# Optimization experiments

Measured on AMD Instinct MI355X. Metric: run time of the kernel, lower is better.

Reference implementation:

```python
import jax, jax.numpy as jnp
import numpy as np

DIM = 1024
HEADS = 16
HEAD_DIM = 64
INNER = HEADS * HEAD_DIM  # 1024
B, N = 4, 2048
EPS = 1e-5


def setup_inputs() -> dict:
    key = jax.random.key(0)
    ks = jax.random.split(key, 5)
    x = jax.random.normal(ks[0], (B, N, DIM), dtype=jnp.float32)
    w_qkv = jax.random.normal(ks[1], (DIM, 3 * INNER), dtype=jnp.float32) * (DIM ** -0.5)
    w_out = jax.random.normal(ks[2], (INNER, DIM), dtype=jnp.float32) * (INNER ** -0.5)
    b_out = jax.random.normal(ks[3], (DIM,), dtype=jnp.float32) * 0.01
    ln_gamma = jnp.ones((DIM,), dtype=jnp.float32)
    ln_beta = jnp.zeros((DIM,), dtype=jnp.float32)
    return {"x": x, "w_qkv": w_qkv, "w_out": w_out, "b_out": b_out,
            "ln_gamma": ln_gamma, "ln_beta": ln_beta}


def reference(x, w_qkv, w_out, b_out, ln_gamma, ln_beta):
    scale = HEAD_DIM ** -0.5
    qkv = x @ w_qkv  # [b, n, 3*inner]
    q, k, v = jnp.split(qkv, 3, axis=-1)
    q = q * scale
    # [b, n, h*d] -> [b, h, n, d]
    def to_heads(t):
        b, n, _ = t.shape
        return t.reshape(b, n, HEADS, HEAD_DIM).transpose(0, 2, 1, 3)
    q, k, v = to_heads(q), to_heads(k), to_heads(v)
    scores = jnp.einsum('bhid,bhjd->bhij', q, k)
    attn = jax.nn.softmax(scores, axis=-1)  # max-subtraction (detached) is internal
    out = jnp.einsum('bhij,bhjd->bhid', attn, v)
    out = out.transpose(0, 2, 1, 3).reshape(x.shape[0], x.shape[1], INNER)
    out = out @ w_out + b_out
    # LayerNorm over last dim
    mu = out.mean(axis=-1, keepdims=True)
    var = out.var(axis=-1, keepdims=True)
    out = (out - mu) * jax.lax.rsqrt(var + EPS)
    return out * ln_gamma + ln_beta
```

## Files before the change

kernel.cpp:

```cpp
#include <hip/hip_runtime.h>


typedef __bf16 bf16;
typedef __bf16 bf16x4 __attribute__((ext_vector_type(4)));
typedef __bf16 bf16x8 __attribute__((ext_vector_type(8)));
typedef float f32x4 __attribute__((ext_vector_type(4)));
typedef float f32x16 __attribute__((ext_vector_type(16)));
typedef unsigned int u32x2 __attribute__((ext_vector_type(2)));
typedef unsigned int u32x4 __attribute__((ext_vector_type(4)));

#define QSCALE_LOG2E 0.18033688011112042f

#define GLOAD_LDS16(gp, lp)                                                   \
  __builtin_amdgcn_global_load_lds(                                           \
      (const __attribute__((address_space(1))) unsigned int*)(const void*)(gp), \
      (__attribute__((address_space(3))) unsigned int*)(void*)(lp), 16, 0, 0)

__device__ __forceinline__ float fexp2(float x) {
#if __has_builtin(__builtin_amdgcn_exp2f)
  return __builtin_amdgcn_exp2f(x);
#else
  return __expf(x * 0.6931471805599453f);
#endif
}

__device__ __forceinline__ unsigned pack2t(float lo, float hi) {
  return __builtin_amdgcn_perm(__float_as_uint(hi), __float_as_uint(lo), 0x07060302u);
}

__global__ __launch_bounds__(256) void cvt_k(const float* __restrict__ in,
                                             bf16* __restrict__ out) {
  const size_t i = ((size_t)blockIdx.x * 256 + threadIdx.x) * 8;
  float4 a = *(const float4*)(in + i);
  float4 b = *(const float4*)(in + i + 4);
  bf16x8 o = {(bf16)a.x, (bf16)a.y, (bf16)a.z, (bf16)a.w,
              (bf16)b.x, (bf16)b.y, (bf16)b.z, (bf16)b.w};
  *(bf16x8*)(out + i) = o;
}

__global__ __launch_bounds__(256) void transpose_k(const float* __restrict__ in,
                                                   bf16* __restrict__ out,
                                                   int Kd, int Nd) {
  __shared__ bf16 t[32][36];
  const int n0 = blockIdx.x * 32, k0 = blockIdx.y * 32;
  const int r = threadIdx.x >> 3, c4 = (threadIdx.x & 7) * 4;
  float4 v = *(const float4*)(in + (size_t)(k0 + r) * Nd + n0 + c4);
  t[c4 + 0][r] = (bf16)v.x; t[c4 + 1][r] = (bf16)v.y;
  t[c4 + 2][r] = (bf16)v.z; t[c4 + 3][r] = (bf16)v.w;
  __syncthreads();
  bf16x4 o = *(const bf16x4*)&t[r][c4];
  *(bf16x4*)(out + (size_t)(n0 + r) * Kd + k0 + c4) = o;
}

template <bool QKV>
__global__ __launch_bounds__(256) void gemm2(const bf16* __restrict__ A,
                                             const bf16* __restrict__ Bt,
                                             bf16* __restrict__ C,
                                             bf16* __restrict__ Vt) {
  __shared__ bf16 As[128][32];
  __shared__ bf16 Bs[128][32];
  const int tid = threadIdx.x;
  const int l = tid & 63, w = tid >> 6;
  const int g = l >> 4, q = l & 15;
  const int wm = w >> 1, wn = w & 1;
  const int m0 = blockIdx.x * 128, n0 = blockIdx.y * 128;
  const int lr = l >> 2, lc = (l & 3) * 8;

  f32x4 acc[4][4] = {};

  for (int k0 = 0; k0 < 1024; k0 += 32) {
    __syncthreads();
#pragma unroll
    for (int i = 0; i < 2; i++) {
      const int c = w + i * 4;
      GLOAD_LDS16(A + (size_t)(m0 + c * 16 + lr) * 1024 + k0 + lc, &As[c * 16][0]);
      GLOAD_LDS16(Bt + (size_t)(n0 + c * 16 + lr) * 1024 + k0 + lc, &Bs[c * 16][0]);
    }
    __syncthreads();

    bf16x8 af[4], bfr[4];
#pragma unroll
    for (int mi = 0; mi < 4; mi++)
      af[mi] = *(const bf16x8*)&As[wm * 64 + mi * 16 + q][g * 8];
#pragma unroll
    for (int ni = 0; ni < 4; ni++)
      bfr[ni] = *(const bf16x8*)&Bs[wn * 64 + ni * 16 + q][g * 8];
#pragma unroll
    for (int mi = 0; mi < 4; mi++)
#pragma unroll
      for (int ni = 0; ni < 4; ni++)
        acc[mi][ni] = __builtin_amdgcn_mfma_f32_16x16x32_bf16(af[mi], bfr[ni], acc[mi][ni], 0, 0, 0);
  }

  if (QKV && n0 >= 2048) {
#pragma unroll
    for (int mi = 0; mi < 4; mi++)
#pragma unroll
      for (int ni = 0; ni < 4; ni++) {
        const int vcol = n0 - 2048 + wn * 64 + ni * 16 + q;
        const int h = vcol >> 6, d = vcol & 63;
        const int t0 = m0 + wm * 64 + mi * 16 + g * 4;
        const int b = t0 >> 11, n = t0 & 2047;
        bf16x4 o = {(bf16)acc[mi][ni][0], (bf16)acc[mi][ni][1],
                    (bf16)acc[mi][ni][2], (bf16)acc[mi][ni][3]};
        *(bf16x4*)(Vt + ((size_t)(b * 16 + h) * 64 + d) * 2048 + n) = o;
      }
  } else {
    const int ldc = QKV ? 2048 : 1024;
    const float s = (QKV && n0 < 1024) ? QSCALE_LOG2E : 1.0f;
#pragma unroll
    for (int mi = 0; mi < 4; mi++)
#pragma unroll
      for (int ni = 0; ni < 4; ni++) {
        const int col = n0 + wn * 64 + ni * 16 + q;
#pragma unroll
        for (int r = 0; r < 4; r++) {
          const int row = m0 + wm * 64 + mi * 16 + g * 4 + r;
          C[(size_t)row * ldc + col] = (bf16)(acc[mi][ni][r] * s);
        }
      }
  }
}

__global__ __launch_bounds__(256, 3) void attn_k(const bf16* __restrict__ qk,
                                                 const bf16* __restrict__ vt,
                                                 bf16* __restrict__ aout) {
  __shared__ bf16 Ks[3][64][64];
  __shared__ bf16 Vs[3][64][64];
  const int tid = threadIdx.x;
  const int l = tid & 63, w = tid >> 6;
  const int q = l & 31, hi = l >> 5, q7 = q & 7;

  const int flat = blockIdx.x;
  const int logical = (flat & 7) * 128 + (flat >> 3);
  const int qt = logical & 15, bh = logical >> 4;
  const int h = bh & 15, b = bh >> 4;
  const int qbase = qt * 128 + w * 32;

  const bf16* Kg = qk + (size_t)(b * 2048) * 2048 + 1024 + h * 64;
  const bf16* Vg = vt + ((size_t)(b * 16 + h) * 64) * 2048;

  bf16x8 qf[4];
  {
    const bf16* Qr = qk + (size_t)(b * 2048 + qbase + q) * 2048 + h * 64 + hi * 8;
#pragma unroll
    for (int i = 0; i < 4; i++) qf[i] = *(const bf16x8*)(Qr + i * 16);
  }

  const int r0 = tid >> 3, sp0 = ((tid & 7) ^ (r0 & 7)) * 8;
  const int ub = (tid >> 6) << 9;
#define STAGE_KV(buf, kt)                                                       \
  do {                                                                          \
    bf16* kd = &Ks[buf][0][0];                                                  \
    bf16* vd = &Vs[buf][0][0];                                                  \
    GLOAD_LDS16(Kg + (size_t)((kt) + r0) * 2048 + sp0, kd + ub);                \
    GLOAD_LDS16(Vg + (size_t)r0 * 2048 + (kt) + sp0, vd + ub);                  \
    GLOAD_LDS16(Kg + (size_t)((kt) + 32 + r0) * 2048 + sp0, kd + 2048 + ub);    \
    GLOAD_LDS16(Vg + (size_t)(32 + r0) * 2048 + (kt) + sp0, vd + 2048 + ub);    \
  } while (0)

  f32x16 oacc[2] = {};
  float lsA = 0.f, lsB = 0.f;

  STAGE_KV(0, 0);
  STAGE_KV(1, 64);
  int cur = 0, nxt2 = 2;

  for (int kt = 0; kt < 2048; kt += 64) {
    if (kt == 2048 - 64) {
      asm volatile("s_waitcnt vmcnt(0)" ::: "memory");
    } else {
      asm volatile("s_waitcnt vmcnt(4)" ::: "memory");
    }
    __builtin_amdgcn_sched_barrier(0);
    __builtin_amdgcn_s_barrier();

    if (kt + 128 < 2048) STAGE_KV(nxt2, kt + 128);

    const char* Kb = (const char*)&Ks[cur][0][0];
    const char* Vb = (const char*)&Vs[cur][0][0];

    f32x16 st[2];
    __builtin_amdgcn_s_setprio(1);
#pragma unroll
    for (int s = 0; s < 2; s++) {
      f32x16 acc = {};
#pragma unroll
      for (int i = 0; i < 4; i++) {
        bf16x8 kf = *(const bf16x8*)(Kb + (s * 32 + q) * 128 + (((2 * i + hi) ^ q7) << 4));
        acc = __builtin_amdgcn_mfma_f32_32x32x16_bf16(kf, qf[i], acc, 0, 0, 0);
      }
      st[s] = acc;
    }
    __builtin_amdgcn_s_setprio(0);

    bf16x8 vfr[2][4];
#pragma unroll
    for (int dblk = 0; dblk < 2; dblk++)
#pragma unroll
      for (int t = 0; t < 4; t++)
        vfr[dblk][t] = *(const bf16x8*)(Vb + (dblk * 32 + q) * 128 + (((2 * t + hi) ^ q7) << 4));

#pragma unroll
    for (int r = 0; r < 16; r++) { st[0][r] = fexp2(st[0][r]); lsA += st[0][r]; }
#pragma unroll
    for (int r = 0; r < 16; r++) { st[1][r] = fexp2(st[1][r]); lsB += st[1][r]; }

    bf16x8 pfrag[4];
#pragma unroll
    for (int s = 0; s < 2; s++)
#pragma unroll
      for (int ks = 0; ks < 2; ks++) {
        const unsigned a0 = pack2t(st[s][8 * ks + 0], st[s][8 * ks + 1]);
        const unsigned a1 = pack2t(st[s][8 * ks + 2], st[s][8 * ks + 3]);
        const unsigned b0 = pack2t(st[s][8 * ks + 4], st[s][8 * ks + 5]);
        const unsigned b1 = pack2t(st[s][8 * ks + 6], st[s][8 * ks + 7]);
        u32x2 w0 = __builtin_amdgcn_permlane32_swap(a0, b0, false, false);
        u32x2 w1 = __builtin_amdgcn_permlane32_swap(a1, b1, false, false);
        u32x4 bw = {w0[0], w1[0], w0[1], w1[1]};
        pfrag[2 * s + ks] = __builtin_bit_cast(bf16x8, bw);
      }

    __builtin_amdgcn_s_setprio(1);
#pragma unroll
    for (int dblk = 0; dblk < 2; dblk++)
#pragma unroll
      for (int t = 0; t < 4; t++)
        oacc[dblk] = __builtin_amdgcn_mfma_f32_32x32x16_bf16(vfr[dblk][t], pfrag[t],
                                                             oacc[dblk], 0, 0, 0);
    __builtin_amdgcn_s_setprio(0);

    cur = (cur == 2) ? 0 : cur + 1;
    nxt2 = (nxt2 == 2) ? 0 : nxt2 + 1;
  }

  float lsum = lsA + lsB;
  {
    u32x2 t2 = __builtin_amdgcn_permlane32_swap(__float_as_uint(lsum),
                                                __float_as_uint(lsum), false, false);
    lsum = __uint_as_float(t2[0]) + __uint_as_float(t2[1]);
  }
  const float inv = 1.f / lsum;
  bf16* orow = aout + (size_t)(b * 2048 + qbase + q) * 1024 + h * 64 + hi * 4;
#pragma unroll
  for (int dblk = 0; dblk < 2; dblk++)
#pragma unroll
    for (int rg = 0; rg < 4; rg++) {
      bf16x4 o = {(bf16)(oacc[dblk][4 * rg + 0] * inv), (bf16)(oacc[dblk][4 * rg + 1] * inv),
                  (bf16)(oacc[dblk][4 * rg + 2] * inv), (bf16)(oacc[dblk][4 * rg + 3] * inv)};
      *(bf16x4*)(orow + dblk * 32 + rg * 8) = o;
    }
#undef STAGE_KV
}

__global__ __launch_bounds__(256) void ln_k(const bf16* __restrict__ proj,
                                            const float* __restrict__ bo,
                                            const float* __restrict__ gam,
                                            const float* __restrict__ bet,
                                            float* __restrict__ out) {
  const int row = blockIdx.x, tid = threadIdx.x;
  const int l = tid & 63, w = tid >> 6;
  bf16x4 pv = *(const bf16x4*)(proj + (size_t)row * 1024 + tid * 4);
  float4 bv = *(const float4*)(bo + tid * 4);
  float v0 = (float)pv[0] + bv.x, v1 = (float)pv[1] + bv.y;
  float v2 = (float)pv[2] + bv.z, v3 = (float)pv[3] + bv.w;
  float s = v0 + v1 + v2 + v3;
  float ss = v0 * v0 + v1 * v1 + v2 * v2 + v3 * v3;
#pragma unroll
  for (int off = 32; off > 0; off >>= 1) {
    s += __shfl_xor(s, off);
    ss += __shfl_xor(ss, off);
  }
  __shared__ float red[8];
  if (l == 0) { red[w] = s; red[w + 4] = ss; }
  __syncthreads();
  const float S = red[0] + red[1] + red[2] + red[3];
  const float SS = red[4] + red[5] + red[6] + red[7];
  const float mean = S * (1.f / 1024.f);
  const float var = SS * (1.f / 1024.f) - mean * mean;
  const float rs = rsqrtf(var + 1e-5f);
  float4 gv = *(const float4*)(gam + tid * 4);
  float4 btv = *(const float4*)(bet + tid * 4);
  float4 o;
  o.x = (v0 - mean) * rs * gv.x + btv.x;
  o.y = (v1 - mean) * rs * gv.y + btv.y;
  o.z = (v2 - mean) * rs * gv.z + btv.z;
  o.w = (v3 - mean) * rs * gv.w + btv.w;
  *(float4*)(out + (size_t)row * 1024 + tid * 4) = o;
}

extern "C" void kernel_launch(void* const* d_in, const int* in_sizes, int n_in,
                              void* d_out, int out_size, void* d_ws, size_t ws_size,
                              hipStream_t stream) {
  const float* x      = (const float*)d_in[0];
  const float* w_qkv  = (const float*)d_in[1];
  const float* w_out  = (const float*)d_in[2];
  const float* b_out  = (const float*)d_in[3];
  const float* gamma  = (const float*)d_in[4];
  const float* beta   = (const float*)d_in[5];
  float* out = (float*)d_out;

  char* ws = (char*)d_ws;
  bf16* xbf   = (bf16*)(ws);
  bf16* wqkvT = (bf16*)(ws + 16777216);
  bf16* woutT = (bf16*)(ws + 23068672);
  bf16* qkbuf = (bf16*)(ws + 25165824);
  bf16* vt    = (bf16*)(ws + 58720256);
  bf16* aout  = xbf;
  bf16* proj  = vt;

  dim3 blk(256);
  cvt_k<<<4096, blk, 0, stream>>>(x, xbf);
  transpose_k<<<dim3(96, 32), blk, 0, stream>>>(w_qkv, wqkvT, 1024, 3072);
  transpose_k<<<dim3(32, 32), blk, 0, stream>>>(w_out, woutT, 1024, 1024);
  gemm2<true><<<dim3(64, 24), blk, 0, stream>>>(xbf, wqkvT, qkbuf, vt);
  attn_k<<<1024, blk, 0, stream>>>(qkbuf, vt, aout);
  gemm2<false><<<dim3(64, 8), blk, 0, stream>>>(aout, woutT, proj, nullptr);
  ln_k<<<8192, blk, 0, stream>>>(proj, b_out, gamma, beta, out);
}
```

Measured before the change: 201.8 us.

## Double-buffer 128-key attention tiles and swizzle GEMM block order across XCDs

```diff
diff --git a/kernel.cpp b/kernel.cpp
--- a/kernel.cpp
+++ b/kernel.cpp
@@ -63,7 +63,10 @@
   const int l = tid & 63, w = tid >> 6;
   const int g = l >> 4, q = l & 15;
   const int wm = w >> 1, wn = w & 1;
-  const int m0 = blockIdx.x * 128, n0 = blockIdx.y * 128;
+  const int nwg = (int)(gridDim.x * gridDim.y);
+  const int flat = (int)(blockIdx.y * gridDim.x + blockIdx.x);
+  const int swz = (flat & 7) * (nwg >> 3) + (flat >> 3);
+  const int m0 = (swz & 63) * 128, n0 = (swz >> 6) * 128;
   const int lr = l >> 2, lc = (l & 3) * 8;
 
   f32x4 acc[4][4] = {};
@@ -125,8 +128,8 @@
 __global__ __launch_bounds__(256, 3) void attn_k(const bf16* __restrict__ qk,
                                                  const bf16* __restrict__ vt,
                                                  bf16* __restrict__ aout) {
-  __shared__ bf16 Ks[3][64][64];
-  __shared__ bf16 Vs[3][64][64];
+  __shared__ bf16 Ks[2][2][64][64];
+  __shared__ bf16 Vs[2][2][64][64];
   const int tid = threadIdx.x;
   const int l = tid & 63, w = tid >> 6;
   const int q = l & 31, hi = l >> 5, q7 = q & 7;
@@ -149,89 +152,88 @@
 
   const int r0 = tid >> 3, sp0 = ((tid & 7) ^ (r0 & 7)) * 8;
   const int ub = (tid >> 6) << 9;
-#define STAGE_KV(buf, kt)                                                       \
+#define STAGE(buf, kt)                                                          \
   do {                                                                          \
-    bf16* kd = &Ks[buf][0][0];                                                  \
-    bf16* vd = &Vs[buf][0][0];                                                  \
-    GLOAD_LDS16(Kg + (size_t)((kt) + r0) * 2048 + sp0, kd + ub);                \
-    GLOAD_LDS16(Vg + (size_t)r0 * 2048 + (kt) + sp0, vd + ub);                  \
-    GLOAD_LDS16(Kg + (size_t)((kt) + 32 + r0) * 2048 + sp0, kd + 2048 + ub);    \
-    GLOAD_LDS16(Vg + (size_t)(32 + r0) * 2048 + (kt) + sp0, vd + 2048 + ub);    \
+    bf16* k0 = &Ks[buf][0][0][0]; bf16* k1 = &Ks[buf][1][0][0];                 \
+    bf16* v0 = &Vs[buf][0][0][0]; bf16* v1 = &Vs[buf][1][0][0];                 \
+    GLOAD_LDS16(Kg + (size_t)((kt) + r0) * 2048 + sp0,           k0 + ub);      \
+    GLOAD_LDS16(Kg + (size_t)((kt) + 32 + r0) * 2048 + sp0,      k0 + 2048 + ub);\
+    GLOAD_LDS16(Kg + (size_t)((kt) + 64 + r0) * 2048 + sp0,      k1 + ub);      \
+    GLOAD_LDS16(Kg + (size_t)((kt) + 96 + r0) * 2048 + sp0,      k1 + 2048 + ub);\
+    GLOAD_LDS16(Vg + (size_t)r0 * 2048 + (kt) + sp0,             v0 + ub);      \
+    GLOAD_LDS16(Vg + (size_t)(32 + r0) * 2048 + (kt) + sp0,      v0 + 2048 + ub);\
+    GLOAD_LDS16(Vg + (size_t)r0 * 2048 + (kt) + 64 + sp0,        v1 + ub);      \
+    GLOAD_LDS16(Vg + (size_t)(32 + r0) * 2048 + (kt) + 64 + sp0, v1 + 2048 + ub);\
   } while (0)
 
   f32x16 oacc[2] = {};
   float lsA = 0.f, lsB = 0.f;
 
-  STAGE_KV(0, 0);
-  STAGE_KV(1, 64);
-  int cur = 0, nxt2 = 2;
-
-  for (int kt = 0; kt < 2048; kt += 64) {
-    if (kt == 2048 - 64) {
-      asm volatile("s_waitcnt vmcnt(0)" ::: "memory");
-    } else {
-      asm volatile("s_waitcnt vmcnt(4)" ::: "memory");
-    }
+#define SUBTILE(Kb, Vb)                                                         \
+  do {                                                                          \
+    f32x16 st[2];                                                               \
+    __builtin_amdgcn_s_setprio(1);                                              \
+    _Pragma("unroll")                                                           \
+    for (int s = 0; s < 2; s++) {                                               \
+      f32x16 acc = {};                                                          \
+      _Pragma("unroll")                                                         \
+      for (int i = 0; i < 4; i++) {                                             \
+        bf16x8 kf = *(const bf16x8*)((Kb) + (s * 32 + q) * 128 +                \
+                                     (((2 * i + hi) ^ q7) << 4));               \
+        acc = __builtin_amdgcn_mfma_f32_32x32x16_bf16(kf, qf[i], acc, 0, 0, 0); \
+      }                                                                         \
+      st[s] = acc;                                                              \
+    }                                                                           \
+    __builtin_amdgcn_s_setprio(0);                                              \
+    bf16x8 vfr[2][4];                                                           \
+    _Pragma("unroll")                                                           \
+    for (int dblk = 0; dblk < 2; dblk++)                                        \
+      _Pragma("unroll")                                                         \
+      for (int t = 0; t < 4; t++)                                               \
+        vfr[dblk][t] = *(const bf16x8*)((Vb) + (dblk * 32 + q) * 128 +          \
+                                        (((2 * t + hi) ^ q7) << 4));            \
+    _Pragma("unroll")                                                           \
+    for (int r = 0; r < 16; r++) { st[0][r] = fexp2(st[0][r]); lsA += st[0][r]; }\
+    _Pragma("unroll")                                                           \
+    for (int r = 0; r < 16; r++) { st[1][r] = fexp2(st[1][r]); lsB += st[1][r]; }\
+    bf16x8 pfrag[4];                                                            \
+    _Pragma("unroll")                                                           \
+    for (int s = 0; s < 2; s++)                                                 \
+      _Pragma("unroll")                                                         \
+      for (int ks = 0; ks < 2; ks++) {                                          \
+        const unsigned a0 = pack2t(st[s][8 * ks + 0], st[s][8 * ks + 1]);       \
+        const unsigned a1 = pack2t(st[s][8 * ks + 2], st[s][8 * ks + 3]);       \
+        const unsigned b0 = pack2t(st[s][8 * ks + 4], st[s][8 * ks + 5]);       \
+        const unsigned b1 = pack2t(st[s][8 * ks + 6], st[s][8 * ks + 7]);       \
+        u32x2 w0 = __builtin_amdgcn_permlane32_swap(a0, b0, false, false);      \
+        u32x2 w1 = __builtin_amdgcn_permlane32_swap(a1, b1, false, false);      \
+        u32x4 bw = {w0[0], w1[0], w0[1], w1[1]};                                \
+        pfrag[2 * s + ks] = __builtin_bit_cast(bf16x8, bw);                     \
+      }                                                                         \
+    __builtin_amdgcn_s_setprio(1);                                              \
+    _Pragma("unroll")                                                           \
+    for (int dblk = 0; dblk < 2; dblk++)                                        \
+      _Pragma("unroll")                                                         \
+      for (int t = 0; t < 4; t++)                                               \
+        oacc[dblk] = __builtin_amdgcn_mfma_f32_32x32x16_bf16(vfr[dblk][t],      \
+                                            pfrag[t], oacc[dblk], 0, 0, 0);     \
+    __builtin_amdgcn_s_setprio(0);                                              \
+  } while (0)
+
+  STAGE(0, 0);
+  int cur = 0;
+
+  for (int kt = 0; kt < 2048; kt += 128) {
+    asm volatile("s_waitcnt vmcnt(0)" ::: "memory");
     __builtin_amdgcn_sched_barrier(0);
     __builtin_amdgcn_s_barrier();
 
-    if (kt + 128 < 2048) STAGE_KV(nxt2, kt + 128);
-
-    const char* Kb = (const char*)&Ks[cur][0][0];
-    const char* Vb = (const char*)&Vs[cur][0][0];
-
-    f32x16 st[2];
-    __builtin_amdgcn_s_setprio(1);
-#pragma unroll
-    for (int s = 0; s < 2; s++) {
-      f32x16 acc = {};
-#pragma unroll
-      for (int i = 0; i < 4; i++) {
-        bf16x8 kf = *(const bf16x8*)(Kb + (s * 32 + q) * 128 + (((2 * i + hi) ^ q7) << 4));
-        acc = __builtin_amdgcn_mfma_f32_32x32x16_bf16(kf, qf[i], acc, 0, 0, 0);
-      }
-      st[s] = acc;
-    }
-    __builtin_amdgcn_s_setprio(0);
-
-    bf16x8 vfr[2][4];
-#pragma unroll
-    for (int dblk = 0; dblk < 2; dblk++)
-#pragma unroll
-      for (int t = 0; t < 4; t++)
-        vfr[dblk][t] = *(const bf16x8*)(Vb + (dblk * 32 + q) * 128 + (((2 * t + hi) ^ q7) << 4));
-
-#pragma unroll
-    for (int r = 0; r < 16; r++) { st[0][r] = fexp2(st[0][r]); lsA += st[0][r]; }
-#pragma unroll
-    for (int r = 0; r < 16; r++) { st[1][r] = fexp2(st[1][r]); lsB += st[1][r]; }
-
-    bf16x8 pfrag[4];
-#pragma unroll
-    for (int s = 0; s < 2; s++)
-#pragma unroll
-      for (int ks = 0; ks < 2; ks++) {
-        const unsigned a0 = pack2t(st[s][8 * ks + 0], st[s][8 * ks + 1]);
-        const unsigned a1 = pack2t(st[s][8 * ks + 2], st[s][8 * ks + 3]);
-        const unsigned b0 = pack2t(st[s][8 * ks + 4], st[s][8 * ks + 5]);
-        const unsigned b1 = pack2t(st[s][8 * ks + 6], st[s][8 * ks + 7]);
-        u32x2 w0 = __builtin_amdgcn_permlane32_swap(a0, b0, false, false);
-        u32x2 w1 = __builtin_amdgcn_permlane32_swap(a1, b1, false, false);
-        u32x4 bw = {w0[0], w1[0], w0[1], w1[1]};
-        pfrag[2 * s + ks] = __builtin_bit_cast(bf16x8, bw);
-      }
-
-    __builtin_amdgcn_s_setprio(1);
-#pragma unroll
-    for (int dblk = 0; dblk < 2; dblk++)
-#pragma unroll
-      for (int t = 0; t < 4; t++)
-        oacc[dblk] = __builtin_amdgcn_mfma_f32_32x32x16_bf16(vfr[dblk][t], pfrag[t],
-                                                             oacc[dblk], 0, 0, 0);
-    __builtin_amdgcn_s_setprio(0);
-
-    cur = (cur == 2) ? 0 : cur + 1;
-    nxt2 = (nxt2 == 2) ? 0 : nxt2 + 1;
+    if (kt + 128 < 2048) STAGE(cur ^ 1, kt + 128);
+
+    SUBTILE((const char*)&Ks[cur][0][0][0], (const char*)&Vs[cur][0][0][0]);
+    SUBTILE((const char*)&Ks[cur][1][0][0], (const char*)&Vs[cur][1][0][0]);
+
+    cur ^= 1;
   }
 
   float lsum = lsA + lsB;
@@ -250,7 +252,8 @@
                   (bf16)(oacc[dblk][4 * rg + 2] * inv), (bf16)(oacc[dblk][4 * rg + 3] * inv)};
       *(bf16x4*)(orow + dblk * 32 + rg * 8) = o;
     }
-#undef STAGE_KV
+#undef SUBTILE
+#undef STAGE
 }
 
 __global__ __launch_bounds__(256) void ln_k(const bf16* __restrict__ proj,
```

New measurement: 215.6 us. 1.07x slower.

## Software-pipeline QK^T of next KV tile with softmax and PV of current

Applied to the files above, without the earlier changes.

```diff
diff --git a/kernel.cpp b/kernel.cpp
--- a/kernel.cpp
+++ b/kernel.cpp
@@ -159,79 +159,104 @@
     GLOAD_LDS16(Vg + (size_t)(32 + r0) * 2048 + (kt) + sp0, vd + 2048 + ub);    \
   } while (0)
 
+#define QKT(buf, sA, sB)                                                        \
+  do {                                                                          \
+    const char* Kb_ = (const char*)&Ks[buf][0][0];                              \
+    __builtin_amdgcn_s_setprio(1);                                              \
+    {                                                                           \
+      f32x16 a_ = {};                                                           \
+      _Pragma("unroll")                                                         \
+      for (int i = 0; i < 4; i++) {                                             \
+        bf16x8 kf = *(const bf16x8*)(Kb_ + q * 128 + (((2 * i + hi) ^ q7) << 4));\
+        a_ = __builtin_amdgcn_mfma_f32_32x32x16_bf16(kf, qf[i], a_, 0, 0, 0);   \
+      }                                                                         \
+      sA = a_;                                                                  \
+    }                                                                           \
+    {                                                                           \
+      f32x16 a_ = {};                                                           \
+      _Pragma("unroll")                                                         \
+      for (int i = 0; i < 4; i++) {                                             \
+        bf16x8 kf = *(const bf16x8*)(Kb_ + (32 + q) * 128 +                     \
+                                     (((2 * i + hi) ^ q7) << 4));               \
+        a_ = __builtin_amdgcn_mfma_f32_32x32x16_bf16(kf, qf[i], a_, 0, 0, 0);   \
+      }                                                                         \
+      sB = a_;                                                                  \
+    }                                                                           \
+    __builtin_amdgcn_s_setprio(0);                                              \
+  } while (0)
+
   f32x16 oacc[2] = {};
   float lsA = 0.f, lsB = 0.f;
 
   STAGE_KV(0, 0);
   STAGE_KV(1, 64);
-  int cur = 0, nxt2 = 2;
-
+  asm volatile("s_waitcnt vmcnt(4)" ::: "memory");
+  __builtin_amdgcn_sched_barrier(0);
+  __builtin_amdgcn_s_barrier();
+
+  f32x16 s0, s1;
+  QKT(0, s0, s1);
+
+  int cur = 0;
   for (int kt = 0; kt < 2048; kt += 64) {
-    if (kt == 2048 - 64) {
-      asm volatile("s_waitcnt vmcnt(0)" ::: "memory");
-    } else {
-      asm volatile("s_waitcnt vmcnt(4)" ::: "memory");
-    }
+    const int nbuf = (cur == 2) ? 0 : cur + 1;
+    const int sbuf = (nbuf == 2) ? 0 : nbuf + 1;
+
+    asm volatile("s_waitcnt vmcnt(0)" ::: "memory");
     __builtin_amdgcn_sched_barrier(0);
     __builtin_amdgcn_s_barrier();
 
-    if (kt + 128 < 2048) STAGE_KV(nxt2, kt + 128);
-
-    const char* Kb = (const char*)&Ks[cur][0][0];
+    if (kt + 128 < 2048) STAGE_KV(sbuf, kt + 128);
+
+    f32x16 n0v, n1v;
+    QKT(nbuf, n0v, n1v);
+
+#pragma unroll
+    for (int r = 0; r < 16; r++) { s0[r] = fexp2(s0[r]); lsA += s0[r]; }
+#pragma unroll
+    for (int r = 0; r < 16; r++) { s1[r] = fexp2(s1[r]); lsB += s1[r]; }
+
+    bf16x8 pfrag[4];
+#pragma unroll
+    for (int ks = 0; ks < 2; ks++) {
+      const unsigned a0 = pack2t(s0[8 * ks + 0], s0[8 * ks + 1]);
+      const unsigned a1 = pack2t(s0[8 * ks + 2], s0[8 * ks + 3]);
+      const unsigned b0 = pack2t(s0[8 * ks + 4], s0[8 * ks + 5]);
+      const unsigned b1 = pack2t(s0[8 * ks + 6], s0[8 * ks + 7]);
+      u32x2 w0 = __builtin_amdgcn_permlane32_swap(a0, b0, false, false);
+      u32x2 w1 = __builtin_amdgcn_permlane32_swap(a1, b1, false, false);
+      u32x4 bw = {w0[0], w1[0], w0[1], w1[1]};
+      pfrag[ks] = __builtin_bit_cast(bf16x8, bw);
+    }
+#pragma unroll
+    for (int ks = 0; ks < 2; ks++) {
+      const unsigned a0 = pack2t(s1[8 * ks + 0], s1[8 * ks + 1]);
+      const unsigned a1 = pack2t(s1[8 * ks + 2], s1[8 * ks + 3]);
+      const unsigned b0 = pack2t(s1[8 * ks + 4], s1[8 * ks + 5]);
+      const unsigned b1 = pack2t(s1[8 * ks + 6], s1[8 * ks + 7]);
+      u32x2 w0 = __builtin_amdgcn_permlane32_swap(a0, b0, false, false);
+      u32x2 w1 = __builtin_amdgcn_permlane32_swap(a1, b1, false, false);
+      u32x4 bw = {w0[0], w1[0], w0[1], w1[1]};
+      pfrag[2 + ks] = __builtin_bit_cast(bf16x8, bw);
+    }
+
     const char* Vb = (const char*)&Vs[cur][0][0];
-
-    f32x16 st[2];
     __builtin_amdgcn_s_setprio(1);
 #pragma unroll
-    for (int s = 0; s < 2; s++) {
-      f32x16 acc = {};
-#pragma unroll
-      for (int i = 0; i < 4; i++) {
-        bf16x8 kf = *(const bf16x8*)(Kb + (s * 32 + q) * 128 + (((2 * i + hi) ^ q7) << 4));
-        acc = __builtin_amdgcn_mfma_f32_32x32x16_bf16(kf, qf[i], acc, 0, 0, 0);
-      }
-      st[s] = acc;
+    for (int dblk = 0; dblk < 2; dblk++) {
+      bf16x8 vfr[4];
+#pragma unroll
+      for (int t = 0; t < 4; t++)
+        vfr[t] = *(const bf16x8*)(Vb + (dblk * 32 + q) * 128 + (((2 * t + hi) ^ q7) << 4));
+#pragma unroll
+      for (int t = 0; t < 4; t++)
+        oacc[dblk] = __builtin_amdgcn_mfma_f32_32x32x16_bf16(vfr[t], pfrag[t],
+                                                             oacc[dblk], 0, 0, 0);
     }
     __builtin_amdgcn_s_setprio(0);
 
-    bf16x8 vfr[2][4];
-#pragma unroll
-    for (int dblk = 0; dblk < 2; dblk++)
-#pragma unroll
-      for (int t = 0; t < 4; t++)
-        vfr[dblk][t] = *(const bf16x8*)(Vb + (dblk * 32 + q) * 128 + (((2 * t + hi) ^ q7) << 4));
-
-#pragma unroll
-    for (int r = 0; r < 16; r++) { st[0][r] = fexp2(st[0][r]); lsA += st[0][r]; }
-#pragma unroll
-    for (int r = 0; r < 16; r++) { st[1][r] = fexp2(st[1][r]); lsB += st[1][r]; }
-
-    bf16x8 pfrag[4];
-#pragma unroll
-    for (int s = 0; s < 2; s++)
-#pragma unroll
-      for (int ks = 0; ks < 2; ks++) {
-        const unsigned a0 = pack2t(st[s][8 * ks + 0], st[s][8 * ks + 1]);
-        const unsigned a1 = pack2t(st[s][8 * ks + 2], st[s][8 * ks + 3]);
-        const unsigned b0 = pack2t(st[s][8 * ks + 4], st[s][8 * ks + 5]);
-        const unsigned b1 = pack2t(st[s][8 * ks + 6], st[s][8 * ks + 7]);
-        u32x2 w0 = __builtin_amdgcn_permlane32_swap(a0, b0, false, false);
-        u32x2 w1 = __builtin_amdgcn_permlane32_swap(a1, b1, false, false);
-        u32x4 bw = {w0[0], w1[0], w0[1], w1[1]};
-        pfrag[2 * s + ks] = __builtin_bit_cast(bf16x8, bw);
-      }
-
-    __builtin_amdgcn_s_setprio(1);
-#pragma unroll
-    for (int dblk = 0; dblk < 2; dblk++)
-#pragma unroll
-      for (int t = 0; t < 4; t++)
-        oacc[dblk] = __builtin_amdgcn_mfma_f32_32x32x16_bf16(vfr[dblk][t], pfrag[t],
-                                                             oacc[dblk], 0, 0, 0);
-    __builtin_amdgcn_s_setprio(0);
-
-    cur = (cur == 2) ? 0 : cur + 1;
-    nxt2 = (nxt2 == 2) ? 0 : nxt2 + 1;
+    s0 = n0v; s1 = n1v;
+    cur = nbuf;
   }
 
   float lsum = lsA + lsB;
@@ -250,6 +275,7 @@
                   (bf16)(oacc[dblk][4 * rg + 2] * inv), (bf16)(oacc[dblk][4 * rg + 3] * inv)};
       *(bf16x4*)(orow + dblk * 32 + rg * 8) = o;
     }
+#undef QKT
 #undef STAGE_KV
 }
 
```

New measurement: 200.5 us (median of 2 runs). No clear change (-0.6%).
